# Kernel tuning notes

Hardware: AMD Instinct MI355X
Metric: run time of the kernel (lower is better)

The kernel has to match this reference:

```python
import jax, jax.numpy as jnp
import numpy as np

HEADS = 8
DIM_HEAD = 64
QUERY_DIM = 512
INNER = HEADS * DIM_HEAD
DIAG_OFFSET = 1
T_TEMP = 1.0
NEG_INF = -1e9  # used via -inf below; kept for clarity


def setup_inputs() -> dict:
    key = jax.random.key(0)
    ks = jax.random.split(key, 8)
    b, s, f = 2, 2048, 16
    x = jax.random.normal(ks[0], (b, s, f, QUERY_DIM), dtype=jnp.float32)
    pos_bias = jax.random.normal(ks[1], (HEADS, f, f), dtype=jnp.float32)
    w_scale = 0.02
    Wq = jax.random.normal(ks[2], (QUERY_DIM, INNER), dtype=jnp.float32) * w_scale
    Wk = jax.random.normal(ks[3], (QUERY_DIM, INNER), dtype=jnp.float32) * w_scale
    Wv = jax.random.normal(ks[4], (QUERY_DIM, INNER), dtype=jnp.float32) * w_scale
    Wo = jax.random.normal(ks[5], (INNER, QUERY_DIM), dtype=jnp.float32) * w_scale
    bo = jax.random.normal(ks[6], (QUERY_DIM,), dtype=jnp.float32) * w_scale
    return {"x": x, "pos_bias": pos_bias, "Wq": Wq, "Wk": Wk, "Wv": Wv, "Wo": Wo, "bo": bo}


def reference(x, pos_bias, Wq, Wk, Wv, Wo, bo):
    # x: [b, s, f, c] -- temporal attention over the frame axis f per spatial token
    b, s, f, _ = x.shape
    scale = DIM_HEAD ** -0.5
    q = (x @ Wq).reshape(b, s, f, HEADS, DIM_HEAD)
    k = (x @ Wk).reshape(b, s, f, HEADS, DIM_HEAD)
    v = (x @ Wv).reshape(b, s, f, HEADS, DIM_HEAD)
    # scores over frames: [b, s, h, f_q, f_k]
    w = jnp.einsum('bsihd,bsjhd->bshij', q * scale, k)
    w = w + pos_bias[None, None]  # [h, f, f] relative position bias
    # attend_prev_only causal mask (strict, diag_offset=1)
    causal = jnp.triu(jnp.ones((f, f), dtype=jnp.float32), k=DIAG_OFFSET)
    w = w + jnp.where(causal == 1.0, -jnp.inf, 0.0)
    # faithful to source: subtract row max, then softmax with temperature
    w = w - jax.lax.stop_gradient(jnp.max(w, axis=-1, keepdims=True))
    p = jax.nn.softmax(w.astype(jnp.float32) / T_TEMP, axis=-1).astype(w.dtype)
    out = jnp.einsum('bshij,bsjhd->bsihd', p, v).reshape(b, s, f, INNER)
    return out @ Wo + bo
```

## Files before the change

kernel.cpp:

```cpp
#include <hip/hip_runtime.h>

typedef unsigned short u16;
typedef __attribute__((ext_vector_type(8))) unsigned short u16x8;
typedef __attribute__((ext_vector_type(8))) __bf16 bf16x8;
typedef __attribute__((ext_vector_type(4))) float f32x4;

#define M_ROWS 65536
#define KDIM   512
#define NKT    8

typedef __attribute__((address_space(1))) const void gconst_void;
typedef __attribute__((address_space(3))) void lds_void;

static __device__ __forceinline__ u16 f2bf(float f) {
  unsigned u = __builtin_bit_cast(unsigned, f);
  u += 0x7FFFu + ((u >> 16) & 1u);
  return (u16)(u >> 16);
}

static __device__ __forceinline__ f32x4 mfma_bf16(u16x8 a, u16x8 b, f32x4 c) {
  return __builtin_amdgcn_mfma_f32_16x16x32_bf16(
      __builtin_bit_cast(bf16x8, a), __builtin_bit_cast(bf16x8, b), c, 0, 0, 0);
}

__global__ void conv_x(const float* __restrict__ x, u16* __restrict__ xb) {
  const size_t t = (size_t)blockIdx.x * 256 + threadIdx.x;
  f32x4 a = *(const f32x4*)(x + t * 8);
  f32x4 b = *(const f32x4*)(x + t * 8 + 4);
  u16x8 w;
#pragma unroll
  for (int e = 0; e < 4; ++e) { w[e] = f2bf(a[e]); w[e + 4] = f2bf(b[e]); }
  *(u16x8*)(xb + t * 8) = w;
}

__global__ void convW_qkv_t(const float* __restrict__ Wq, const float* __restrict__ Wk,
                            const float* __restrict__ Wv, u16* __restrict__ Wt) {
  __shared__ float tile[32][33];
  const int bn = blockIdx.x * 32;
  const int bk = blockIdx.y * 32;
  const int tx = threadIdx.x & 31, ty = threadIdx.x >> 5;
  const float* W = (bn < 512) ? Wq : ((bn < 1024) ? Wk : Wv);
  const int coln = bn & 511;
#pragma unroll
  for (int r = 0; r < 32; r += 8)
    tile[ty + r][tx] = W[(size_t)(bk + ty + r) * 512 + coln + tx];
  __syncthreads();
#pragma unroll
  for (int r = 0; r < 32; r += 8)
    Wt[(size_t)(bn + ty + r) * 512 + bk + tx] = f2bf(tile[tx][ty + r]);
}

__global__ void convWo_t(const float* __restrict__ Wo, u16* __restrict__ Wt) {
  __shared__ float tile[32][33];
  const int bn = blockIdx.x * 32;
  const int bk = blockIdx.y * 32;
  const int tx = threadIdx.x & 31, ty = threadIdx.x >> 5;
#pragma unroll
  for (int r = 0; r < 32; r += 8)
    tile[ty + r][tx] = Wo[(size_t)(bk + ty + r) * 512 + bn + tx];
  __syncthreads();
#pragma unroll
  for (int r = 0; r < 32; r += 8)
    Wt[(size_t)(bn + ty + r) * 512 + bk + tx] = f2bf(tile[tx][ty + r]);
}

__global__ __launch_bounds__(512, 2)
void gemm_qkv_attn(const u16* __restrict__ A, const u16* __restrict__ Wt,
                   const float* __restrict__ pos_bias, u16* __restrict__ attnbuf) {
  __shared__ __attribute__((aligned(16))) u16 smem[73728];
  u16* Ab   = smem;
  u16* Bb   = smem + 49152;
  u16* qkvT = smem;
  u16* Pl   = smem + 51200;

  const int tid  = threadIdx.x;
  const int lane = tid & 63;
  const int wid  = tid >> 6;
  const int wm   = wid >> 1;
  const int wn   = wid & 1;
  const int lg   = lane >> 4;
  const int lc   = lane & 15;
  const int srow = lane >> 3;
  const int sg   = (lane & 7) ^ srow;

  const int nwg  = gridDim.x;
  const int cpx  = nwg >> 3;
  const int flat = blockIdx.x;
  const int swz  = (flat & 7) * cpx + (flat >> 3);
  const int mt   = swz >> 3;
  const int h    = swz & 7;
  const int row0 = mt * 256;

  auto stageA = [&](int buf, int unit, int kt) {
    const int rl = unit * 64 + wid * 8;
    const u16* src = A + (size_t)(row0 + rl + srow) * KDIM + kt * 64 + sg * 8;
    __builtin_amdgcn_global_load_lds((gconst_void*)src,
                                     (lds_void*)&Ab[buf * 16384 + rl * 64], 16, 0, 0);
  };
  auto stageB = [&](int buf, int unit, int kt) {
    const int rl = unit * 64 + wid * 8;
    const int grow = unit * 512 + h * 64 + wid * 8 + srow;
    const u16* src = Wt + (size_t)grow * KDIM + kt * 64 + sg * 8;
    __builtin_amdgcn_global_load_lds((gconst_void*)src,
                                     (lds_void*)&Bb[buf * 12288 + rl * 64], 16, 0, 0);
  };

  f32x4 acc[4][6];
#pragma unroll
  for (int mi = 0; mi < 4; ++mi)
#pragma unroll
    for (int ni = 0; ni < 6; ++ni) acc[mi][ni] = (f32x4){0.f, 0.f, 0.f, 0.f};

#pragma unroll
  for (int u = 0; u < 4; ++u) stageA(0, u, 0);
#pragma unroll
  for (int u = 0; u < 3; ++u) stageB(0, u, 0);
#pragma unroll
  for (int u = 0; u < 4; ++u) stageA(1, u, 1);

  for (int t = 0; t < NKT; ++t) {
    const int  ab   = t % 3;
    const int  bb   = t & 1;
    const bool preB = (t + 1) < NKT;
    const bool preA = (t + 2) < NKT;
    const int  ab2  = (t + 2) % 3;

    if (t < NKT - 1) asm volatile("s_waitcnt vmcnt(4)" ::: "memory");
    else             asm volatile("s_waitcnt vmcnt(0)" ::: "memory");
    __builtin_amdgcn_s_barrier();

    u16x8 af[2], bfr[6];
#pragma unroll
    for (int ph = 0; ph < 4; ++ph) {
      const int ks = ph >> 1;
      const int mh = ph & 1;
      const int gsw = ((ks * 4 + lg) ^ (lc & 7)) << 3;
      if (mh == 0) {
#pragma unroll
        for (int ni = 0; ni < 6; ++ni)
          bfr[ni] = *(const u16x8*)&Bb[bb * 12288 + (wn * 96 + ni * 16 + lc) * 64 + gsw];
      }
#pragma unroll
      for (int i = 0; i < 2; ++i)
        af[i] = *(const u16x8*)&Ab[ab * 16384 + (wm * 64 + (mh * 2 + i) * 16 + lc) * 64 + gsw];

      if (ph == 0 && preB) { stageB(bb ^ 1, 0, t + 1); stageB(bb ^ 1, 1, t + 1); }
      if (ph == 1) { if (preB) stageB(bb ^ 1, 2, t + 1); if (preA) stageA(ab2, 0, t + 2); }
      if (ph == 2 && preA) { stageA(ab2, 1, t + 2); stageA(ab2, 2, t + 2); }
      if (ph == 3 && preA) { stageA(ab2, 3, t + 2); }

      __builtin_amdgcn_s_barrier();
      asm volatile("s_waitcnt lgkmcnt(0)" ::: "memory");
      __builtin_amdgcn_sched_barrier(0);
      __builtin_amdgcn_s_setprio(1);
#pragma unroll
      for (int i = 0; i < 2; ++i)
#pragma unroll
        for (int ni = 0; ni < 6; ++ni)
          acc[mh * 2 + i][ni] = mfma_bf16(af[i], bfr[ni], acc[mh * 2 + i][ni]);
      __builtin_amdgcn_s_setprio(0);
      __builtin_amdgcn_sched_barrier(0);
      if (ph < 3) __builtin_amdgcn_s_barrier();
    }
  }
  __syncthreads();

#pragma unroll
  for (int mi = 0; mi < 4; ++mi)
#pragma unroll
    for (int ni = 0; ni < 6; ++ni) {
      const int col = wn * 96 + ni * 16 + lc;
      const int rb  = wm * 64 + mi * 16 + lg * 4;
#pragma unroll
      for (int r = 0; r < 4; ++r)
        qkvT[(rb + r) * 200 + col] = f2bf(acc[mi][ni][r]);
    }
  __syncthreads();

  const float scale = 0.125f;
  const f32x4 zf = {0.f, 0.f, 0.f, 0.f};
#pragma unroll
  for (int tt = 0; tt < 2; ++tt) {
    const int tok = wid * 2 + tt;
    const int rb  = tok * 16;
    const int qb  = (rb + lc) * 200;

    u16x8 aq0 = *(const u16x8*)&qkvT[qb + 0  + lg * 8];
    u16x8 aq1 = *(const u16x8*)&qkvT[qb + 32 + lg * 8];
    u16x8 bk0 = *(const u16x8*)&qkvT[qb + 64 + lg * 8];
    u16x8 bk1 = *(const u16x8*)&qkvT[qb + 96 + lg * 8];
    f32x4 s = mfma_bf16(aq0, bk0, zf);
    s = mfma_bf16(aq1, bk1, s);

    const int pb = wid * 512 + tt * 256;
#pragma unroll
    for (int r = 0; r < 4; ++r) {
      const int i = lg * 4 + r;
      float sv = s[r] * scale + pos_bias[h * 256 + i * 16 + lc];
      if (lc > i) sv = -1e30f;
      float m = sv;
#pragma unroll
      for (int off = 8; off >= 1; off >>= 1) m = fmaxf(m, __shfl_xor(m, off));
      float e = __expf(sv - m);
      float sm = e;
#pragma unroll
      for (int off = 8; off >= 1; off >>= 1) sm += __shfl_xor(sm, off);
      Pl[pb + i * 16 + lc] = f2bf(e / sm);
    }
    asm volatile("s_waitcnt lgkmcnt(0)" ::: "memory");

    u16x8 ap = {0, 0, 0, 0, 0, 0, 0, 0};
    if (lane < 32) ap = *(const u16x8*)&Pl[pb + lc * 16 + lg * 8];

#pragma unroll
    for (int nd = 0; nd < 4; ++nd) {
      u16x8 bv = {0, 0, 0, 0, 0, 0, 0, 0};
      if (lane < 32) {
#pragma unroll
        for (int jj = 0; jj < 8; ++jj) {
          const int j = lg * 8 + jj;
          bv[jj] = qkvT[(rb + j) * 200 + 128 + nd * 16 + lc];
        }
      }
      f32x4 o = mfma_bf16(ap, bv, zf);
#pragma unroll
      for (int r = 0; r < 4; ++r) {
        const int i = lg * 4 + r;
        attnbuf[(size_t)(row0 + rb + i) * 512 + h * 64 + nd * 16 + lc] = f2bf(o[r]);
      }
    }
  }
}

__global__ __launch_bounds__(512, 2)
void gemm_out(const u16* __restrict__ A, const u16* __restrict__ Bt,
              float* __restrict__ C, const float* __restrict__ bias) {
  __shared__ __attribute__((aligned(16))) u16 smem[65536];
  u16* Ab = smem;
  u16* Bb = smem + 49152;

  const int tid  = threadIdx.x;
  const int lane = tid & 63;
  const int wid  = tid >> 6;
  const int wm   = wid >> 1;
  const int wn   = wid & 1;
  const int lg   = lane >> 4;
  const int lc   = lane & 15;
  const int srow = lane >> 3;
  const int sg   = (lane & 7) ^ srow;

  const int nwg  = gridDim.x;
  const int cpx  = nwg >> 3;
  const int flat = blockIdx.x;
  const int swz  = (flat & 7) * cpx + (flat >> 3);
  const int mt   = swz >> 2;
  const int nt   = swz & 3;
  const int row0 = mt * 256, col0 = nt * 128;

  auto stageA = [&](int buf, int unit, int kt) {
    const int rl = unit * 64 + wid * 8;
    const u16* src = A + (size_t)(row0 + rl + srow) * KDIM + kt * 64 + sg * 8;
    __builtin_amdgcn_global_load_lds((gconst_void*)src,
                                     (lds_void*)&Ab[buf * 16384 + rl * 64], 16, 0, 0);
  };
  auto stageB = [&](int buf, int unit, int kt) {
    const int rl = unit * 64 + wid * 8;
    const u16* src = Bt + (size_t)(col0 + rl + srow) * KDIM + kt * 64 + sg * 8;
    __builtin_amdgcn_global_load_lds((gconst_void*)src,
                                     (lds_void*)&Bb[buf * 8192 + rl * 64], 16, 0, 0);
  };

  f32x4 acc[4][4];
#pragma unroll
  for (int mi = 0; mi < 4; ++mi)
#pragma unroll
    for (int ni = 0; ni < 4; ++ni) acc[mi][ni] = (f32x4){0.f, 0.f, 0.f, 0.f};

#pragma unroll
  for (int u = 0; u < 4; ++u) stageA(0, u, 0);
#pragma unroll
  for (int u = 0; u < 2; ++u) stageB(0, u, 0);
#pragma unroll
  for (int u = 0; u < 4; ++u) stageA(1, u, 1);

  for (int t = 0; t < NKT; ++t) {
    const int  ab   = t % 3;
    const int  bb   = t & 1;
    const bool preB = (t + 1) < NKT;
    const bool preA = (t + 2) < NKT;
    const int  ab2  = (t + 2) % 3;

    if (t < NKT - 1) asm volatile("s_waitcnt vmcnt(4)" ::: "memory");
    else             asm volatile("s_waitcnt vmcnt(0)" ::: "memory");
    __builtin_amdgcn_s_barrier();

    u16x8 af[2], bfr[4];
#pragma unroll
    for (int ph = 0; ph < 4; ++ph) {
      const int ks = ph >> 1;
      const int mh = ph & 1;
      const int gsw = ((ks * 4 + lg) ^ (lc & 7)) << 3;
      if (mh == 0) {
#pragma unroll
        for (int ni = 0; ni < 4; ++ni)
          bfr[ni] = *(const u16x8*)&Bb[bb * 8192 + (wn * 64 + ni * 16 + lc) * 64 + gsw];
      }
#pragma unroll
      for (int i = 0; i < 2; ++i)
        af[i] = *(const u16x8*)&Ab[ab * 16384 + (wm * 64 + (mh * 2 + i) * 16 + lc) * 64 + gsw];

      if (ph == 0 && preB) { stageB(bb ^ 1, 0, t + 1); stageB(bb ^ 1, 1, t + 1); }
      if (ph == 1 && preA) { stageA(ab2, 0, t + 2); stageA(ab2, 1, t + 2); }
      if (ph == 2 && preA) { stageA(ab2, 2, t + 2); stageA(ab2, 3, t + 2); }

      __builtin_amdgcn_s_barrier();
      asm volatile("s_waitcnt lgkmcnt(0)" ::: "memory");
      __builtin_amdgcn_sched_barrier(0);
      __builtin_amdgcn_s_setprio(1);
#pragma unroll
      for (int i = 0; i < 2; ++i)
#pragma unroll
        for (int ni = 0; ni < 4; ++ni)
          acc[mh * 2 + i][ni] = mfma_bf16(af[i], bfr[ni], acc[mh * 2 + i][ni]);
      __builtin_amdgcn_s_setprio(0);
      __builtin_amdgcn_sched_barrier(0);
      if (ph < 3) __builtin_amdgcn_s_barrier();
    }
  }

  const int gmb = row0 + wm * 64;
  const int gnb = col0 + wn * 64;
#pragma unroll
  for (int mi = 0; mi < 4; ++mi)
#pragma unroll
    for (int ni = 0; ni < 4; ++ni) {
      const int gm = gmb + mi * 16 + lg * 4;
      const int gn = gnb + ni * 16 + lc;
      const float bv = bias[gn];
      f32x4 v = acc[mi][ni];
#pragma unroll
      for (int r = 0; r < 4; ++r) C[(size_t)(gm + r) * 512 + gn] = v[r] + bv;
    }
}

extern "C" void kernel_launch(void* const* d_in, const int* in_sizes, int n_in,
                              void* d_out, int out_size, void* d_ws, size_t ws_size,
                              hipStream_t stream) {
  const float* x        = (const float*)d_in[0];
  const float* pos_bias = (const float*)d_in[1];
  const float* Wq       = (const float*)d_in[2];
  const float* Wk       = (const float*)d_in[3];
  const float* Wv       = (const float*)d_in[4];
  const float* Wo       = (const float*)d_in[5];
  const float* bo       = (const float*)d_in[6];
  float* out            = (float*)d_out;

  u16* xb      = (u16*)d_ws;
  u16* attnbuf = xb + (size_t)M_ROWS * 512;
  u16* Wo_t    = attnbuf + (size_t)M_ROWS * 512;
  u16* Wqkv_t  = (u16*)d_out;

  conv_x<<<dim3(M_ROWS * KDIM / (256 * 8)), dim3(256), 0, stream>>>(x, xb);
  convW_qkv_t<<<dim3(48, 16), dim3(256), 0, stream>>>(Wq, Wk, Wv, Wqkv_t);
  gemm_qkv_attn<<<dim3(2048), dim3(512), 0, stream>>>(xb, Wqkv_t, pos_bias, attnbuf);
  convWo_t<<<dim3(16, 16), dim3(256), 0, stream>>>(Wo, Wo_t);
  gemm_out<<<dim3(1024), dim3(512), 0, stream>>>(attnbuf, Wo_t, out, bo);
}
```

Baseline: 224.3 us.

## Replace four-phase barrier-interleaved GEMM mainloop with bulk prefetch and two k-steps

In both the fused QKV/attention kernel and the output projection kernel, the per-tile mainloop no longer uses four phases separated by s_barrier, setprio and sched_barrier. All global-to-LDS staging for the next tiles is now issued at the start of the iteration, then two k-substeps each load every A/B fragment and run all MFMAs. This removes several workgroup barriers per tile and leaves instruction interleaving to the compiler. In exchange it loses the explicit MFMA/load overlap and priority hints, and raises register pressure from holding four A fragments at once.

```diff
diff --git a/kernel.cpp b/kernel.cpp
--- a/kernel.cpp
+++ b/kernel.cpp
@@ -129,38 +129,25 @@
     else             asm volatile("s_waitcnt vmcnt(0)" ::: "memory");
     __builtin_amdgcn_s_barrier();
 
-    u16x8 af[2], bfr[6];
-#pragma unroll
-    for (int ph = 0; ph < 4; ++ph) {
-      const int ks = ph >> 1;
-      const int mh = ph & 1;
+    if (preB) { stageB(bb ^ 1, 0, t + 1); stageB(bb ^ 1, 1, t + 1); stageB(bb ^ 1, 2, t + 1); }
+    if (preA) { stageA(ab2, 0, t + 2); stageA(ab2, 1, t + 2);
+                stageA(ab2, 2, t + 2); stageA(ab2, 3, t + 2); }
+
+#pragma unroll
+    for (int ks = 0; ks < 2; ++ks) {
       const int gsw = ((ks * 4 + lg) ^ (lc & 7)) << 3;
-      if (mh == 0) {
+      u16x8 bfr[6], af[4];
+#pragma unroll
+      for (int ni = 0; ni < 6; ++ni)
+        bfr[ni] = *(const u16x8*)&Bb[bb * 12288 + (wn * 96 + ni * 16 + lc) * 64 + gsw];
+#pragma unroll
+      for (int i = 0; i < 4; ++i)
+        af[i] = *(const u16x8*)&Ab[ab * 16384 + (wm * 64 + i * 16 + lc) * 64 + gsw];
+#pragma unroll
+      for (int i = 0; i < 4; ++i)
 #pragma unroll
         for (int ni = 0; ni < 6; ++ni)
-          bfr[ni] = *(const u16x8*)&Bb[bb * 12288 + (wn * 96 + ni * 16 + lc) * 64 + gsw];
-      }
-#pragma unroll
-      for (int i = 0; i < 2; ++i)
-        af[i] = *(const u16x8*)&Ab[ab * 16384 + (wm * 64 + (mh * 2 + i) * 16 + lc) * 64 + gsw];
-
-      if (ph == 0 && preB) { stageB(bb ^ 1, 0, t + 1); stageB(bb ^ 1, 1, t + 1); }
-      if (ph == 1) { if (preB) stageB(bb ^ 1, 2, t + 1); if (preA) stageA(ab2, 0, t + 2); }
-      if (ph == 2 && preA) { stageA(ab2, 1, t + 2); stageA(ab2, 2, t + 2); }
-      if (ph == 3 && preA) { stageA(ab2, 3, t + 2); }
-
-      __builtin_amdgcn_s_barrier();
-      asm volatile("s_waitcnt lgkmcnt(0)" ::: "memory");
-      __builtin_amdgcn_sched_barrier(0);
-      __builtin_amdgcn_s_setprio(1);
-#pragma unroll
-      for (int i = 0; i < 2; ++i)
-#pragma unroll
-        for (int ni = 0; ni < 6; ++ni)
-          acc[mh * 2 + i][ni] = mfma_bf16(af[i], bfr[ni], acc[mh * 2 + i][ni]);
-      __builtin_amdgcn_s_setprio(0);
-      __builtin_amdgcn_sched_barrier(0);
-      if (ph < 3) __builtin_amdgcn_s_barrier();
+          acc[i][ni] = mfma_bf16(af[i], bfr[ni], acc[i][ni]);
     }
   }
   __syncthreads();
@@ -294,37 +281,25 @@
     else             asm volatile("s_waitcnt vmcnt(0)" ::: "memory");
     __builtin_amdgcn_s_barrier();
 
-    u16x8 af[2], bfr[4];
-#pragma unroll
-    for (int ph = 0; ph < 4; ++ph) {
-      const int ks = ph >> 1;
-      const int mh = ph & 1;
+    if (preB) { stageB(bb ^ 1, 0, t + 1); stageB(bb ^ 1, 1, t + 1); }
+    if (preA) { stageA(ab2, 0, t + 2); stageA(ab2, 1, t + 2);
+                stageA(ab2, 2, t + 2); stageA(ab2, 3, t + 2); }
+
+#pragma unroll
+    for (int ks = 0; ks < 2; ++ks) {
       const int gsw = ((ks * 4 + lg) ^ (lc & 7)) << 3;
-      if (mh == 0) {
+      u16x8 bfr[4], af[4];
+#pragma unroll
+      for (int ni = 0; ni < 4; ++ni)
+        bfr[ni] = *(const u16x8*)&Bb[bb * 8192 + (wn * 64 + ni * 16 + lc) * 64 + gsw];
+#pragma unroll
+      for (int i = 0; i < 4; ++i)
+        af[i] = *(const u16x8*)&Ab[ab * 16384 + (wm * 64 + i * 16 + lc) * 64 + gsw];
+#pragma unroll
+      for (int i = 0; i < 4; ++i)
 #pragma unroll
         for (int ni = 0; ni < 4; ++ni)
-          bfr[ni] = *(const u16x8*)&Bb[bb * 8192 + (wn * 64 + ni * 16 + lc) * 64 + gsw];
-      }
-#pragma unroll
-      for (int i = 0; i < 2; ++i)
-        af[i] = *(const u16x8*)&Ab[ab * 16384 + (wm * 64 + (mh * 2 + i) * 16 + lc) * 64 + gsw];
-
-      if (ph == 0 && preB) { stageB(bb ^ 1, 0, t + 1); stageB(bb ^ 1, 1, t + 1); }
-      if (ph == 1 && preA) { stageA(ab2, 0, t + 2); stageA(ab2, 1, t + 2); }
-      if (ph == 2 && preA) { stageA(ab2, 2, t + 2); stageA(ab2, 3, t + 2); }
-
-      __builtin_amdgcn_s_barrier();
-      asm volatile("s_waitcnt lgkmcnt(0)" ::: "memory");
-      __builtin_amdgcn_sched_barrier(0);
-      __builtin_amdgcn_s_setprio(1);
-#pragma unroll
-      for (int i = 0; i < 2; ++i)
-#pragma unroll
-        for (int ni = 0; ni < 4; ++ni)
-          acc[mh * 2 + i][ni] = mfma_bf16(af[i], bfr[ni], acc[mh * 2 + i][ni]);
-      __builtin_amdgcn_s_setprio(0);
-      __builtin_amdgcn_sched_barrier(0);
-      if (ph < 3) __builtin_amdgcn_s_barrier();
+          acc[i][ni] = mfma_bf16(af[i], bfr[ni], acc[i][ni]);
     }
   }
 
```

Result: no change. 220.6 us (-1.6%).
